# Performance work log

Hardware: AMD Instinct MI355X
Metric: run time of the kernel (lower is better)

Reference implementation:

```python
import jax, jax.numpy as jnp
import numpy as np

B, H, W, N = 8, 384, 384, 96
STEPSZ = 0.1; ALPHA = 0.01; BETA = 0.01; STD = 1.0
NSTEPS = 50; NSTEPS_W = 10; DMAX = 15.0; EXTGRADFAC = 10.0

def make_gauss_edge_fltr(std):
    # Gaussian-derivative edge filters, one per spatial dim: [2,1,k,k]
    r = int(np.ceil(3 * std)); t = np.arange(-r, r + 1, dtype=np.float32)
    g = np.exp(-t * t / (2 * std * std)); g /= g.sum()
    dg = -t / (std * std) * np.exp(-t * t / (2 * std * std)); dg /= np.abs(dg).sum()
    fy = np.outer(dg, g)   # d/drow
    fx = np.outer(g, dg)   # d/dcol
    return np.stack([fy, fx])[:, None].astype(np.float32)

def setup_inputs() -> dict:
    key = jax.random.key(0)
    k1, k2 = jax.random.split(key, 2)
    pred_dmap = jax.random.normal(k1, (B, 1, H, W), jnp.float32)
    nodes = jax.random.uniform(k2, (B, N, 2), jnp.float32)
    nodes = nodes * jnp.array([H - 1.0, W - 1.0], jnp.float32)
    nodes = jnp.sort(nodes, axis=1)  # roughly monotone chain -> path-like snake
    widths = jnp.ones((B, N), jnp.float32) * 3.0
    fltr = jnp.asarray(make_gauss_edge_fltr(STD))
    return {"pred_dmap": pred_dmap, "nodes": nodes, "widths": widths, "fltr": fltr}

def grad_im(x, fltr):
    # x: [B,1,H,W], fltr: [2,1,k,k] -> [B,2,H,W]
    return jax.lax.conv_general_dilated(x, fltr, (1, 1), 'SAME',
                                        dimension_numbers=('NCHW', 'OIHW', 'NCHW'))

def interp(img, pts):
    # bilinear sample: img [C,H,W], pts [N,2] (row,col) -> [N,C]
    C, Hh, Ww = img.shape
    y = jnp.clip(pts[:, 0], 0.0, Hh - 1.0); x = jnp.clip(pts[:, 1], 0.0, Ww - 1.0)
    y0 = jnp.floor(y).astype(jnp.int32); x0 = jnp.floor(x).astype(jnp.int32)
    y1 = jnp.minimum(y0 + 1, Hh - 1); x1 = jnp.minimum(x0 + 1, Ww - 1)
    wy = y - y0; wx = x - x0
    v00 = img[:, y0, x0]; v01 = img[:, y0, x1]
    v10 = img[:, y1, x0]; v11 = img[:, y1, x1]
    v = v00 * (1 - wy) * (1 - wx) + v01 * (1 - wy) * wx + v10 * wy * (1 - wx) + v11 * wy * wx
    return v.T

def d2_open(x):
    # second difference with replicated endpoints (open snake)
    xp = jnp.concatenate([x[:1], x, x[-1:]], 0)
    return xp[:-2] - 2 * xp[1:-1] + xp[2:]

def snake_one(nodes, widths, g, gw):
    # explicit active-contour iterations on node positions
    def pstep(x, _):
        fext = interp(g, x)                       # [N,2] external force
        d2 = d2_open(x); d4 = d2_open(d2)
        return x + STEPSZ * (ALPHA * d2 - BETA * d4 + fext), None
    x, _ = jax.lax.scan(pstep, nodes, None, length=NSTEPS)
    # unit normals from central-difference tangents
    t = jnp.concatenate([x[1:2] - x[0:1], 0.5 * (x[2:] - x[:-2]), x[-1:] - x[-2:-1]], 0)
    n = jnp.stack([-t[:, 1], t[:, 0]], 1)
    n = n / (jnp.linalg.norm(n, axis=1, keepdims=True) + 1e-6)
    def wstep(w, _):
        gp = interp(gw, x + w[:, None] * n); gm = interp(gw, x - w[:, None] * n)
        f = 0.5 * (jnp.sum(gp * n, 1) - jnp.sum(gm * n, 1))
        return jnp.maximum(w + STEPSZ * f, 0.5), None
    w, _ = jax.lax.scan(wstep, widths, None, length=NSTEPS_W)
    return x, w

def render(x, w):
    # distance-to-ribbon map, clipped at DMAX; only [HW,S] intermediates
    ys, xs = jnp.meshgrid(jnp.arange(H, dtype=jnp.float32),
                          jnp.arange(W, dtype=jnp.float32), indexing='ij')
    P = jnp.stack([ys.ravel(), xs.ravel()], 1)          # [HW,2]
    a = x[:-1]; ab = x[1:] - a                          # [S,2]
    denom = jnp.sum(ab * ab, 1) + 1e-8                  # [S]
    dotpa = P @ ab.T - jnp.sum(a * ab, 1)               # [HW,S] = (P-a).ab
    t = jnp.clip(dotpa / denom, 0.0, 1.0)
    pa2 = jnp.sum(P * P, 1)[:, None] - 2 * (P @ a.T) + jnp.sum(a * a, 1)  # |P-a|^2
    d = jnp.sqrt(jnp.maximum(pa2 - 2 * t * dotpa + t * t * denom, 0.0))
    ws = 0.5 * (w[:-1] + w[1:])                         # per-segment width
    dmap = jnp.min(jnp.maximum(d - ws, 0.0), axis=1)
    return jnp.minimum(dmap, DMAX).reshape(H, W)

def reference(pred_dmap, nodes, widths, fltr):
    gimg = grad_im(pred_dmap, fltr) * EXTGRADFAC          # [B,2,H,W]
    gimgW = grad_im(jnp.abs(pred_dmap), fltr) * EXTGRADFAC
    def per_sample(nd, wd, g, gw):
        x, w = snake_one(nd, wd, g, gw)
        return render(x, w)
    dm = jax.vmap(per_sample)(nodes, widths, gimg, gimgW)[:, None]  # [B,1,H,W]
    dm = jax.lax.stop_gradient(dm)   # snake_dm.detach() in the original
    return jnp.mean((pred_dmap - dm) ** 2)
```

## Files before the change

kernel.cpp:

```cpp
#include <hip/hip_runtime.h>
#include <math.h>

#define BB   8
#define HH   384
#define WW   384
#define NN   96
#define HWSZ (HH * WW)
#define NSEG (NN - 1)
#define SEGF 12
#define DMAXV 15.0f

__global__ __launch_bounds__(256) void conv_kernel(
    const float* __restrict__ pred, const float* __restrict__ fltr,
    float* __restrict__ g, float* __restrict__ gw)
{
    __shared__ float sf[98];
    int tid = threadIdx.x;
    if (tid < 98) sf[tid] = fltr[tid];
    __syncthreads();

    int gidx = blockIdx.x * 256 + tid;
    int b = gidx / HWSZ;
    int p = gidx - b * HWSZ;
    int y = p / WW;
    int x = p - y * WW;
    const float* pb = pred + b * HWSZ;

    float a0 = 0.f, a1 = 0.f, a2 = 0.f, a3 = 0.f;
#pragma unroll
    for (int ky = 0; ky < 7; ++ky) {
        int iy = y + ky - 3;
        bool oky = (iy >= 0) && (iy < HH);
        const float* row = pb + iy * WW;
#pragma unroll
        for (int kx = 0; kx < 7; ++kx) {
            int ix = x + kx - 3;
            float v = (oky && ix >= 0 && ix < WW) ? row[ix] : 0.0f;
            float f0 = sf[ky * 7 + kx];
            float f1 = sf[49 + ky * 7 + kx];
            float av = fabsf(v);
            a0 = fmaf(v,  f0, a0);
            a1 = fmaf(v,  f1, a1);
            a2 = fmaf(av, f0, a2);
            a3 = fmaf(av, f1, a3);
        }
    }
    float* gb  = g  + b * 2 * HWSZ;
    float* gwb = gw + b * 2 * HWSZ;
    gb[p]         = a0 * 10.0f;
    gb[HWSZ + p]  = a1 * 10.0f;
    gwb[p]        = a2 * 10.0f;
    gwb[HWSZ + p] = a3 * 10.0f;
}

__device__ inline void bilin2(const float* __restrict__ img, float py, float px,
                              float& v0, float& v1)
{
    float y = fminf(fmaxf(py, 0.0f), (float)(HH - 1));
    float x = fminf(fmaxf(px, 0.0f), (float)(WW - 1));
    int y0 = (int)floorf(y);
    int x0 = (int)floorf(x);
    int y1 = min(y0 + 1, HH - 1);
    int x1 = min(x0 + 1, WW - 1);
    float wy = y - (float)y0;
    float wx = x - (float)x0;
    float w00 = (1.f - wy) * (1.f - wx);
    float w01 = (1.f - wy) * wx;
    float w10 = wy * (1.f - wx);
    float w11 = wy * wx;
    const float* c0 = img;
    const float* c1 = img + HWSZ;
    int i00 = y0 * WW + x0, i01 = y0 * WW + x1, i10 = y1 * WW + x0, i11 = y1 * WW + x1;
    v0 = c0[i00] * w00 + c0[i01] * w01 + c0[i10] * w10 + c0[i11] * w11;
    v1 = c1[i00] * w00 + c1[i01] * w01 + c1[i10] * w10 + c1[i11] * w11;
}

__global__ __launch_bounds__(128) void snake_kernel(
    const float* __restrict__ nodes, const float* __restrict__ widths,
    const float* __restrict__ g, const float* __restrict__ gw,
    float* __restrict__ segs)
{
    __shared__ float sx[2][2][NN];
    __shared__ float sd2[2][NN];
    __shared__ float swd[NN];

    int b = blockIdx.x;
    int i = threadIdx.x;
    const float* gb  = g  + b * 2 * HWSZ;
    const float* gwb = gw + b * 2 * HWSZ;

    float xy = 0.f, xx = 0.f;
    if (i < NN) {
        xy = nodes[(b * NN + i) * 2 + 0];
        xx = nodes[(b * NN + i) * 2 + 1];
        sx[0][0][i] = xy;
        sx[0][1][i] = xx;
    }
    __syncthreads();

    int il = (i > 0) ? i - 1 : 0;
    int ir = (i < NN - 1) ? i + 1 : NN - 1;
    int cur = 0;

    for (int s = 0; s < 50; ++s) {
        float d2y = 0.f, d2x = 0.f;
        if (i < NN) {
            d2y = sx[cur][0][il] - 2.0f * xy + sx[cur][0][ir];
            d2x = sx[cur][1][il] - 2.0f * xx + sx[cur][1][ir];
            sd2[0][i] = d2y;
            sd2[1][i] = d2x;
        }
        __syncthreads();
        if (i < NN) {
            float d4y = sd2[0][il] - 2.0f * d2y + sd2[0][ir];
            float d4x = sd2[1][il] - 2.0f * d2x + sd2[1][ir];
            float f0, f1;
            bilin2(gb, xy, xx, f0, f1);
            xy = xy + 0.1f * (0.01f * d2y - 0.01f * d4y + f0);
            xx = xx + 0.1f * (0.01f * d2x - 0.01f * d4x + f1);
            sx[1 - cur][0][i] = xy;
            sx[1 - cur][1][i] = xx;
        }
        __syncthreads();
        cur = 1 - cur;
    }

    float ny = 0.f, nx = 0.f;
    if (i < NN) {
        float ty, tx;
        if (i == 0)           { ty = sx[cur][0][1] - xy;            tx = sx[cur][1][1] - xx; }
        else if (i == NN - 1) { ty = xy - sx[cur][0][NN - 2];       tx = xx - sx[cur][1][NN - 2]; }
        else                  { ty = 0.5f * (sx[cur][0][i + 1] - sx[cur][0][i - 1]);
                                tx = 0.5f * (sx[cur][1][i + 1] - sx[cur][1][i - 1]); }
        float n0 = -tx, n1 = ty;
        float nrm = sqrtf(n0 * n0 + n1 * n1) + 1e-6f;
        ny = n0 / nrm;
        nx = n1 / nrm;
    }

    float w = 0.f;
    if (i < NN) w = widths[b * NN + i];
    for (int s = 0; s < 10; ++s) {
        if (i < NN) {
            float p0, p1, m0, m1;
            bilin2(gwb, xy + w * ny, xx + w * nx, p0, p1);
            bilin2(gwb, xy - w * ny, xx - w * nx, m0, m1);
            float f = 0.5f * ((p0 * ny + p1 * nx) - (m0 * ny + m1 * nx));
            w = fmaxf(w + 0.1f * f, 0.5f);
        }
    }
    if (i < NN) swd[i] = w;
    __syncthreads();

    if (i < NSEG) {
        float by = sx[cur][0][i + 1], bx = sx[cur][1][i + 1];
        float aby = by - xy, abx = bx - xx;
        float denom = aby * aby + abx * abx + 1e-8f;
        float aab = xy * aby + xx * abx;
        float aa  = xy * xy + xx * xx;
        float wseg = 0.5f * (w + swd[i + 1]);
        float ymin = fminf(xy, by), ymax = fmaxf(xy, by);
        float reach = DMAXV + wseg;
        float* r = segs + (b * NSEG + i) * SEGF;
        r[0]  = xy;   r[1]  = xx;
        r[2]  = aby;  r[3]  = abx;
        r[4]  = aab;  r[5]  = denom;
        r[6]  = 1.0f / denom;
        r[7]  = aa;   r[8]  = wseg;
        r[9]  = ymin - reach;
        r[10] = ymax + reach;
        r[11] = 0.f;
    }
}

__global__ __launch_bounds__(384) void render_kernel(
    const float* __restrict__ pred, const float* __restrict__ segs,
    float* __restrict__ partials)
{
    __shared__ float ss[NSEG * SEGF];
    __shared__ int slo, shi;
    __shared__ float swsum[6];

    int b = blockIdx.x / HH;
    int y = blockIdx.x - b * HH;
    int t = threadIdx.x;

    const float* sb = segs + b * NSEG * SEGF;
    for (int j = t; j < NSEG * SEGF; j += 384) ss[j] = sb[j];
    if (t == 0) { slo = NSEG; shi = -1; }
    __syncthreads();

    float py = (float)y;
    if (t < NSEG) {
        float ylo = ss[t * SEGF + 9];
        float yhi = ss[t * SEGF + 10];
        if (py >= ylo && py <= yhi) {
            atomicMin(&slo, t);
            atomicMax(&shi, t);
        }
    }
    __syncthreads();

    float px = (float)t;
    float pp = py * py + px * px;
    float minv = DMAXV;

    int lo = slo, hi = shi;
    for (int si = lo; si <= hi; ++si) {
        const float* r = ss + si * SEGF;
        float dotpa = fmaf(py, r[2], fmaf(px, r[3], -r[4]));
        float tt = fminf(fmaxf(dotpa * r[6], 0.0f), 1.0f);
        float pa2 = fmaf(py, -2.0f * r[0], fmaf(px, -2.0f * r[1], pp + r[7]));
        float d2 = fmaf(tt, fmaf(tt, r[5], -2.0f * dotpa), pa2);
        float d = sqrtf(fmaxf(d2, 0.0f));
        float v = fmaxf(d - r[8], 0.0f);
        minv = fminf(minv, v);
    }

    float pr = pred[b * HWSZ + y * WW + t];
    float diff = pr - minv;
    float sq = diff * diff;

#pragma unroll
    for (int off = 32; off > 0; off >>= 1) sq += __shfl_down(sq, off, 64);
    if ((t & 63) == 0) swsum[t >> 6] = sq;
    __syncthreads();
    if (t == 0) {
        float tot = swsum[0] + swsum[1] + swsum[2] + swsum[3] + swsum[4] + swsum[5];
        partials[blockIdx.x] = tot;
    }
}

__global__ __launch_bounds__(1024) void finalize_kernel(
    const float* __restrict__ partials, float* __restrict__ out)
{
    __shared__ float sred[16];
    int t = threadIdx.x;
    float s = 0.f;
    for (int j = t; j < BB * HH; j += 1024) s += partials[j];
#pragma unroll
    for (int off = 32; off > 0; off >>= 1) s += __shfl_down(s, off, 64);
    if ((t & 63) == 0) sred[t >> 6] = s;
    __syncthreads();
    if (t == 0) {
        float tot = 0.f;
        for (int k = 0; k < 16; ++k) tot += sred[k];
        out[0] = tot * (1.0f / (float)(BB * HWSZ));
    }
}

extern "C" void kernel_launch(void* const* d_in, const int* in_sizes, int n_in,
                              void* d_out, int out_size, void* d_ws, size_t ws_size,
                              hipStream_t stream)
{
    const float* pred   = (const float*)d_in[0];
    const float* nodes  = (const float*)d_in[1];
    const float* widths = (const float*)d_in[2];
    const float* fltr   = (const float*)d_in[3];
    float* out = (float*)d_out;

    float* ws       = (float*)d_ws;
    float* g        = ws;
    float* gw       = g  + (size_t)BB * 2 * HWSZ;
    float* segs     = gw + (size_t)BB * 2 * HWSZ;
    float* partials = segs + (size_t)BB * NSEG * SEGF;

    conv_kernel<<<(BB * HWSZ) / 256, 256, 0, stream>>>(pred, fltr, g, gw);
    snake_kernel<<<BB, 128, 0, stream>>>(nodes, widths, g, gw, segs);
    render_kernel<<<BB * HH, 384, 0, stream>>>(pred, segs, partials);
    finalize_kernel<<<1, 1024, 0, stream>>>(partials, out);
}
```

Measured before the change: 142.5 us.

## Interleave gradient channels, run snake in one wavefront, fuse final reduction

Result: slower. 212.5 us (+49.1%).

```diff
diff --git a/kernel.cpp b/kernel.cpp
--- a/kernel.cpp
+++ b/kernel.cpp
@@ -12,7 +12,7 @@
 
 __global__ __launch_bounds__(256) void conv_kernel(
     const float* __restrict__ pred, const float* __restrict__ fltr,
-    float* __restrict__ g, float* __restrict__ gw)
+    float* __restrict__ g2, float* __restrict__ gw2)
 {
     __shared__ float sf[98];
     int tid = threadIdx.x;
@@ -27,34 +27,49 @@
     const float* pb = pred + b * HWSZ;
 
     float a0 = 0.f, a1 = 0.f, a2 = 0.f, a3 = 0.f;
-#pragma unroll
-    for (int ky = 0; ky < 7; ++ky) {
-        int iy = y + ky - 3;
-        bool oky = (iy >= 0) && (iy < HH);
-        const float* row = pb + iy * WW;
-#pragma unroll
-        for (int kx = 0; kx < 7; ++kx) {
-            int ix = x + kx - 3;
-            float v = (oky && ix >= 0 && ix < WW) ? row[ix] : 0.0f;
-            float f0 = sf[ky * 7 + kx];
-            float f1 = sf[49 + ky * 7 + kx];
-            float av = fabsf(v);
-            a0 = fmaf(v,  f0, a0);
-            a1 = fmaf(v,  f1, a1);
-            a2 = fmaf(av, f0, a2);
-            a3 = fmaf(av, f1, a3);
-        }
-    }
-    float* gb  = g  + b * 2 * HWSZ;
-    float* gwb = gw + b * 2 * HWSZ;
-    gb[p]         = a0 * 10.0f;
-    gb[HWSZ + p]  = a1 * 10.0f;
-    gwb[p]        = a2 * 10.0f;
-    gwb[HWSZ + p] = a3 * 10.0f;
-}
-
-__device__ inline void bilin2(const float* __restrict__ img, float py, float px,
-                              float& v0, float& v1)
+    if (y >= 3 && y < HH - 3 && x >= 3 && x < WW - 3) {
+        const float* base = pb + (y - 3) * WW + (x - 3);
+#pragma unroll
+        for (int ky = 0; ky < 7; ++ky) {
+#pragma unroll
+            for (int kx = 0; kx < 7; ++kx) {
+                float v  = base[ky * WW + kx];
+                float f0 = sf[ky * 7 + kx];
+                float f1 = sf[49 + ky * 7 + kx];
+                float av = fabsf(v);
+                a0 = fmaf(v,  f0, a0);
+                a1 = fmaf(v,  f1, a1);
+                a2 = fmaf(av, f0, a2);
+                a3 = fmaf(av, f1, a3);
+            }
+        }
+    } else {
+#pragma unroll
+        for (int ky = 0; ky < 7; ++ky) {
+            int iy = y + ky - 3;
+            bool oky = (iy >= 0) && (iy < HH);
+            const float* row = pb + iy * WW;
+#pragma unroll
+            for (int kx = 0; kx < 7; ++kx) {
+                int ix = x + kx - 3;
+                float v = (oky && ix >= 0 && ix < WW) ? row[ix] : 0.0f;
+                float f0 = sf[ky * 7 + kx];
+                float f1 = sf[49 + ky * 7 + kx];
+                float av = fabsf(v);
+                a0 = fmaf(v,  f0, a0);
+                a1 = fmaf(v,  f1, a1);
+                a2 = fmaf(av, f0, a2);
+                a3 = fmaf(av, f1, a3);
+            }
+        }
+    }
+    float2* gb  = (float2*)g2  + (size_t)b * HWSZ;
+    float2* gwb = (float2*)gw2 + (size_t)b * HWSZ;
+    gb[p]  = make_float2(a0 * 10.0f, a1 * 10.0f);
+    gwb[p] = make_float2(a2 * 10.0f, a3 * 10.0f);
+}
+
+__device__ inline float2 bilin2i(const float2* __restrict__ img, float py, float px)
 {
     float y = fminf(fmaxf(py, 0.0f), (float)(HH - 1));
     float x = fminf(fmaxf(px, 0.0f), (float)(WW - 1));
@@ -64,118 +79,128 @@
     int x1 = min(x0 + 1, WW - 1);
     float wy = y - (float)y0;
     float wx = x - (float)x0;
+    float2 v00 = img[y0 * WW + x0];
+    float2 v01 = img[y0 * WW + x1];
+    float2 v10 = img[y1 * WW + x0];
+    float2 v11 = img[y1 * WW + x1];
     float w00 = (1.f - wy) * (1.f - wx);
     float w01 = (1.f - wy) * wx;
     float w10 = wy * (1.f - wx);
     float w11 = wy * wx;
-    const float* c0 = img;
-    const float* c1 = img + HWSZ;
-    int i00 = y0 * WW + x0, i01 = y0 * WW + x1, i10 = y1 * WW + x0, i11 = y1 * WW + x1;
-    v0 = c0[i00] * w00 + c0[i01] * w01 + c0[i10] * w10 + c0[i11] * w11;
-    v1 = c1[i00] * w00 + c1[i01] * w01 + c1[i10] * w10 + c1[i11] * w11;
-}
-
-__global__ __launch_bounds__(128) void snake_kernel(
+    return make_float2(v00.x * w00 + v01.x * w01 + v10.x * w10 + v11.x * w11,
+                       v00.y * w00 + v01.y * w01 + v10.y * w10 + v11.y * w11);
+}
+
+__device__ inline void write_seg(float* __restrict__ r,
+                                 float py, float px, float qy, float qx, float wseg)
+{
+    float aby = qy - py, abx = qx - px;
+    float denom = aby * aby + abx * abx + 1e-8f;
+    float aab = py * aby + px * abx;
+    float aa  = py * py + px * px;
+    float reach = DMAXV + wseg;
+    r[0]  = py;   r[1]  = px;
+    r[2]  = aby;  r[3]  = abx;
+    r[4]  = aab;  r[5]  = denom;
+    r[6]  = 1.0f / denom;
+    r[7]  = aa;   r[8]  = wseg;
+    r[9]  = fminf(py, qy) - reach;
+    r[10] = fmaxf(py, qy) + reach;
+    r[11] = 0.f;
+}
+
+__global__ __launch_bounds__(64) void snake_kernel(
     const float* __restrict__ nodes, const float* __restrict__ widths,
-    const float* __restrict__ g, const float* __restrict__ gw,
-    float* __restrict__ segs)
-{
-    __shared__ float sx[2][2][NN];
-    __shared__ float sd2[2][NN];
-    __shared__ float swd[NN];
-
+    const float* __restrict__ g2, const float* __restrict__ gw2,
+    float* __restrict__ segs, float* __restrict__ accum,
+    unsigned int* __restrict__ counter)
+{
     int b = blockIdx.x;
-    int i = threadIdx.x;
-    const float* gb  = g  + b * 2 * HWSZ;
-    const float* gwb = gw + b * 2 * HWSZ;
-
-    float xy = 0.f, xx = 0.f;
-    if (i < NN) {
-        xy = nodes[(b * NN + i) * 2 + 0];
-        xx = nodes[(b * NN + i) * 2 + 1];
-        sx[0][0][i] = xy;
-        sx[0][1][i] = xx;
-    }
-    __syncthreads();
-
-    int il = (i > 0) ? i - 1 : 0;
-    int ir = (i < NN - 1) ? i + 1 : NN - 1;
-    int cur = 0;
+    int t = threadIdx.x;
+    if (b == 0 && t == 0) { *accum = 0.f; *counter = 0u; }
+
+    const float2* gb  = (const float2*)g2  + (size_t)b * HWSZ;
+    const float2* gwb = (const float2*)gw2 + (size_t)b * HWSZ;
+    const int HALF = NN / 2;
+    bool act = (t < HALF);
+
+    float ay = 0.f, ax = 0.f, by = 0.f, bx = 0.f;
+    if (act) {
+        const float* np = nodes + (size_t)(b * NN + 2 * t) * 2;
+        ay = np[0]; ax = np[1]; by = np[2]; bx = np[3];
+    }
 
     for (int s = 0; s < 50; ++s) {
-        float d2y = 0.f, d2x = 0.f;
-        if (i < NN) {
-            d2y = sx[cur][0][il] - 2.0f * xy + sx[cur][0][ir];
-            d2x = sx[cur][1][il] - 2.0f * xx + sx[cur][1][ir];
-            sd2[0][i] = d2y;
-            sd2[1][i] = d2x;
-        }
-        __syncthreads();
-        if (i < NN) {
-            float d4y = sd2[0][il] - 2.0f * d2y + sd2[0][ir];
-            float d4x = sd2[1][il] - 2.0f * d2x + sd2[1][ir];
-            float f0, f1;
-            bilin2(gb, xy, xx, f0, f1);
-            xy = xy + 0.1f * (0.01f * d2y - 0.01f * d4y + f0);
-            xx = xx + 0.1f * (0.01f * d2x - 0.01f * d4x + f1);
-            sx[1 - cur][0][i] = xy;
-            sx[1 - cur][1][i] = xx;
-        }
-        __syncthreads();
-        cur = 1 - cur;
-    }
-
-    float ny = 0.f, nx = 0.f;
-    if (i < NN) {
-        float ty, tx;
-        if (i == 0)           { ty = sx[cur][0][1] - xy;            tx = sx[cur][1][1] - xx; }
-        else if (i == NN - 1) { ty = xy - sx[cur][0][NN - 2];       tx = xx - sx[cur][1][NN - 2]; }
-        else                  { ty = 0.5f * (sx[cur][0][i + 1] - sx[cur][0][i - 1]);
-                                tx = 0.5f * (sx[cur][1][i + 1] - sx[cur][1][i - 1]); }
-        float n0 = -tx, n1 = ty;
-        float nrm = sqrtf(n0 * n0 + n1 * n1) + 1e-6f;
-        ny = n0 / nrm;
-        nx = n1 / nrm;
-    }
-
-    float w = 0.f;
-    if (i < NN) w = widths[b * NN + i];
-    for (int s = 0; s < 10; ++s) {
-        if (i < NN) {
-            float p0, p1, m0, m1;
-            bilin2(gwb, xy + w * ny, xx + w * nx, p0, p1);
-            bilin2(gwb, xy - w * ny, xx - w * nx, m0, m1);
-            float f = 0.5f * ((p0 * ny + p1 * nx) - (m0 * ny + m1 * nx));
-            w = fmaxf(w + 0.1f * f, 0.5f);
-        }
-    }
-    if (i < NN) swd[i] = w;
-    __syncthreads();
-
-    if (i < NSEG) {
-        float by = sx[cur][0][i + 1], bx = sx[cur][1][i + 1];
-        float aby = by - xy, abx = bx - xx;
-        float denom = aby * aby + abx * abx + 1e-8f;
-        float aab = xy * aby + xx * abx;
-        float aa  = xy * xy + xx * xx;
-        float wseg = 0.5f * (w + swd[i + 1]);
-        float ymin = fminf(xy, by), ymax = fmaxf(xy, by);
-        float reach = DMAXV + wseg;
-        float* r = segs + (b * NSEG + i) * SEGF;
-        r[0]  = xy;   r[1]  = xx;
-        r[2]  = aby;  r[3]  = abx;
-        r[4]  = aab;  r[5]  = denom;
-        r[6]  = 1.0f / denom;
-        r[7]  = aa;   r[8]  = wseg;
-        r[9]  = ymin - reach;
-        r[10] = ymax + reach;
-        r[11] = 0.f;
+        float2 fa = bilin2i(gb, ay, ax);
+        float2 fb = bilin2i(gb, by, bx);
+
+        float bLy = __shfl_up(by, 1, 64), bLx = __shfl_up(bx, 1, 64);
+        float aRy = __shfl_down(ay, 1, 64), aRx = __shfl_down(ax, 1, 64);
+        bLy = (t == 0) ? ay : bLy;  bLx = (t == 0) ? ax : bLx;
+        aRy = (t == HALF - 1) ? by : aRy;  aRx = (t == HALF - 1) ? bx : aRx;
+
+        float d2ay = bLy - 2.f * ay + by,  d2ax = bLx - 2.f * ax + bx;
+        float d2by = ay  - 2.f * by + aRy, d2bx = ax  - 2.f * bx + aRx;
+
+        float d2bLy = __shfl_up(d2by, 1, 64), d2bLx = __shfl_up(d2bx, 1, 64);
+        float d2aRy = __shfl_down(d2ay, 1, 64), d2aRx = __shfl_down(d2ax, 1, 64);
+        d2bLy = (t == 0) ? d2ay : d2bLy;  d2bLx = (t == 0) ? d2ax : d2bLx;
+        d2aRy = (t == HALF - 1) ? d2by : d2aRy;  d2aRx = (t == HALF - 1) ? d2bx : d2aRx;
+
+        float d4ay = d2bLy - 2.f * d2ay + d2by,  d4ax = d2bLx - 2.f * d2ax + d2bx;
+        float d4by = d2ay  - 2.f * d2by + d2aRy, d4bx = d2ax  - 2.f * d2bx + d2aRx;
+
+        ay += 0.1f * (0.01f * d2ay - 0.01f * d4ay + fa.x);
+        ax += 0.1f * (0.01f * d2ax - 0.01f * d4ax + fa.y);
+        by += 0.1f * (0.01f * d2by - 0.01f * d4by + fb.x);
+        bx += 0.1f * (0.01f * d2bx - 0.01f * d4bx + fb.y);
+    }
+
+    {
+        float bLy = __shfl_up(by, 1, 64), bLx = __shfl_up(bx, 1, 64);
+        float aRy = __shfl_down(ay, 1, 64), aRx = __shfl_down(ax, 1, 64);
+        float tay = 0.5f * (by - bLy), tax = 0.5f * (bx - bLx);
+        if (t == 0) { tay = by - ay; tax = bx - ax; }
+        float tby = 0.5f * (aRy - ay), tbx = 0.5f * (aRx - ax);
+        if (t == HALF - 1) { tby = by - ay; tbx = bx - ax; }
+
+        float na0 = -tax, na1 = tay;
+        float nrm = sqrtf(na0 * na0 + na1 * na1) + 1e-6f;
+        float nay = na0 / nrm, nax = na1 / nrm;
+        float nb0 = -tbx, nb1 = tby;
+        nrm = sqrtf(nb0 * nb0 + nb1 * nb1) + 1e-6f;
+        float nby = nb0 / nrm, nbx = nb1 / nrm;
+
+        float wa = 0.f, wb = 0.f;
+        if (act) { wa = widths[b * NN + 2 * t]; wb = widths[b * NN + 2 * t + 1]; }
+        for (int s = 0; s < 10; ++s) {
+            float2 pa = bilin2i(gwb, ay + wa * nay, ax + wa * nax);
+            float2 ma = bilin2i(gwb, ay - wa * nay, ax - wa * nax);
+            float2 pb = bilin2i(gwb, by + wb * nby, bx + wb * nbx);
+            float2 mb = bilin2i(gwb, by - wb * nby, bx - wb * nbx);
+            float fa = 0.5f * ((pa.x * nay + pa.y * nax) - (ma.x * nay + ma.y * nax));
+            float fb = 0.5f * ((pb.x * nby + pb.y * nbx) - (mb.x * nby + mb.y * nbx));
+            wa = fmaxf(wa + 0.1f * fa, 0.5f);
+            wb = fmaxf(wb + 0.1f * fb, 0.5f);
+        }
+
+        float aRy2 = __shfl_down(ay, 1, 64), aRx2 = __shfl_down(ax, 1, 64);
+        float waR  = __shfl_down(wa, 1, 64);
+        if (act) {
+            float* r0 = segs + (size_t)(b * NSEG + 2 * t) * SEGF;
+            write_seg(r0, ay, ax, by, bx, 0.5f * (wa + wb));
+            if (t < HALF - 1) {
+                float* r1 = segs + (size_t)(b * NSEG + 2 * t + 1) * SEGF;
+                write_seg(r1, by, bx, aRy2, aRx2, 0.5f * (wb + waR));
+            }
+        }
     }
 }
 
 __global__ __launch_bounds__(384) void render_kernel(
     const float* __restrict__ pred, const float* __restrict__ segs,
-    float* __restrict__ partials)
+    float* __restrict__ accum, unsigned int* __restrict__ counter,
+    float* __restrict__ out)
 {
     __shared__ float ss[NSEG * SEGF];
     __shared__ int slo, shi;
@@ -185,7 +210,7 @@
     int y = blockIdx.x - b * HH;
     int t = threadIdx.x;
 
-    const float* sb = segs + b * NSEG * SEGF;
+    const float* sb = segs + (size_t)b * NSEG * SEGF;
     for (int j = t; j < NSEG * SEGF; j += 384) ss[j] = sb[j];
     if (t == 0) { slo = NSEG; shi = -1; }
     __syncthreads();
@@ -217,7 +242,7 @@
         minv = fminf(minv, v);
     }
 
-    float pr = pred[b * HWSZ + y * WW + t];
+    float pr = pred[(size_t)b * HWSZ + y * WW + t];
     float diff = pr - minv;
     float sq = diff * diff;
 
@@ -227,25 +252,13 @@
     __syncthreads();
     if (t == 0) {
         float tot = swsum[0] + swsum[1] + swsum[2] + swsum[3] + swsum[4] + swsum[5];
-        partials[blockIdx.x] = tot;
-    }
-}
-
-__global__ __launch_bounds__(1024) void finalize_kernel(
-    const float* __restrict__ partials, float* __restrict__ out)
-{
-    __shared__ float sred[16];
-    int t = threadIdx.x;
-    float s = 0.f;
-    for (int j = t; j < BB * HH; j += 1024) s += partials[j];
-#pragma unroll
-    for (int off = 32; off > 0; off >>= 1) s += __shfl_down(s, off, 64);
-    if ((t & 63) == 0) sred[t >> 6] = s;
-    __syncthreads();
-    if (t == 0) {
-        float tot = 0.f;
-        for (int k = 0; k < 16; ++k) tot += sred[k];
-        out[0] = tot * (1.0f / (float)(BB * HWSZ));
+        atomicAdd(accum, tot);
+        __threadfence();
+        unsigned int done = atomicAdd(counter, 1u);
+        if (done == (unsigned int)(BB * HH - 1)) {
+            float total = atomicAdd(accum, 0.0f);
+            out[0] = total * (1.0f / (float)(BB * HWSZ));
+        }
     }
 }
 
@@ -259,14 +272,14 @@
     const float* fltr   = (const float*)d_in[3];
     float* out = (float*)d_out;
 
-    float* ws       = (float*)d_ws;
-    float* g        = ws;
-    float* gw       = g  + (size_t)BB * 2 * HWSZ;
-    float* segs     = gw + (size_t)BB * 2 * HWSZ;
-    float* partials = segs + (size_t)BB * NSEG * SEGF;
-
-    conv_kernel<<<(BB * HWSZ) / 256, 256, 0, stream>>>(pred, fltr, g, gw);
-    snake_kernel<<<BB, 128, 0, stream>>>(nodes, widths, g, gw, segs);
-    render_kernel<<<BB * HH, 384, 0, stream>>>(pred, segs, partials);
-    finalize_kernel<<<1, 1024, 0, stream>>>(partials, out);
-}
+    float* ws   = (float*)d_ws;
+    float* g2   = ws;
+    float* gw2  = g2 + (size_t)BB * 2 * HWSZ;
+    float* segs = gw2 + (size_t)BB * 2 * HWSZ;
+    float* accum = segs + (size_t)BB * NSEG * SEGF;
+    unsigned int* counter = (unsigned int*)(accum + 1);
+
+    conv_kernel<<<(BB * HWSZ) / 256, 256, 0, stream>>>(pred, fltr, g2, gw2);
+    snake_kernel<<<BB, 64, 0, stream>>>(nodes, widths, g2, gw2, segs, accum, counter);
+    render_kernel<<<BB * HH, 384, 0, stream>>>(pred, segs, accum, counter, out);
+}
```
